# Performance work log

Hardware: AMD Instinct MI355X
Metric: run time of the kernel (lower is better)

The kernel has to match this reference:

```python
import jax, jax.numpy as jnp
import numpy as np
from jax import lax

V, E, H = 32000, 512, 1024  # vocab, embedding_dim, hidden_dim
S, B, T = 50, 64, 10        # src len, batch, max decode steps
SOS = 0


def setup_inputs() -> dict:
    key = jax.random.key(0)
    ks = jax.random.split(key, 16)
    sc = 0.02
    n = jax.random.normal
    return {
        "enc_out": n(ks[0], (S, B, 2 * H), jnp.float32),
        "hidden": n(ks[1], (1, B, H), jnp.float32),
        "target": jax.random.randint(ks[2], (B, T), 0, V),
        "emb": n(ks[3], (V, E), jnp.float32) * sc,
        "w_ih": n(ks[4], (3 * H, E), jnp.float32) * sc,
        "w_hh": n(ks[5], (3 * H, H), jnp.float32) * sc,
        "b_ih": n(ks[6], (3 * H,), jnp.float32) * sc,
        "b_hh": n(ks[7], (3 * H,), jnp.float32) * sc,
        "wa_w": n(ks[8], (H, H), jnp.float32) * sc,
        "wa_b": n(ks[9], (H,), jnp.float32) * sc,
        "ua_w": n(ks[10], (H, 2 * H), jnp.float32) * sc,
        "ua_b": n(ks[11], (H,), jnp.float32) * sc,
        "va_w": n(ks[12], (1, H), jnp.float32) * sc,
        "va_b": n(ks[13], (1,), jnp.float32) * sc,
    }


def reference(enc_out, hidden, target, emb, w_ih, w_hh, b_ih, b_hh,
              wa_w, wa_b, ua_w, ua_b, va_w, va_b):
    b, t = target.shape

    def gru_cell(x, h):
        gi = x @ w_ih.T + b_ih          # [B, 3H]
        gh = h @ w_hh.T + b_hh          # [B, 3H]
        ir, iz, inn = jnp.split(gi, 3, axis=-1)
        hr, hz, hn = jnp.split(gh, 3, axis=-1)
        r = jax.nn.sigmoid(ir + hr)
        z = jax.nn.sigmoid(iz + hz)
        nng = jnp.tanh(inn + r * hn)
        return (1.0 - z) * nng + z * h

    # teacher-forced decoder inputs: [SOS, target[:, :-1]] -> [T, B]
    dec_in = jnp.concatenate(
        [jnp.full((b, 1), SOS, dtype=target.dtype), target[:, : t - 1]], axis=1)
    xs = emb[dec_in].transpose(1, 0, 2)  # [T, B, E] (dropout is identity in eval)

    def step(h, x):
        h2 = gru_cell(x, h)
        return h2, h2

    h_last, hs = lax.scan(step, hidden[0], xs)   # hs: [T, B, H]

    keys = enc_out.transpose(1, 0, 2)            # [B, S, 2H]
    uk = keys @ ua_w.T + ua_b                    # [B, S, H]
    wq = hs @ wa_w.T + wa_b                      # [T, B, H]
    # additive (Bahdanau) scores: [T, B, S]
    scores = (jnp.tanh(wq[:, :, None, :] + uk[None]) @ va_w.T + va_b)[..., 0]
    weights = jax.nn.softmax(scores, axis=-1)    # over source positions
    context = jnp.einsum('tbs,bsd->btd', weights, keys)  # [B, T, 2H]
    out = jax.nn.log_softmax(context, axis=-1)   # [B, T, 2H]
    return out, h_last
```

## Files before the change

### kernel.cpp

```cpp
#include <hip/hip_runtime.h>
#include <math.h>

#define VOCAB 32000
#define E_DIM 512
#define H_DIM 1024
#define S_LEN 50
#define B_SZ 64
#define T_LEN 10
#define H3 (3 * H_DIM)
#define D2H (2 * H_DIM)

typedef __attribute__((ext_vector_type(8))) short short8;
typedef __attribute__((ext_vector_type(4))) float floatx4;

__device__ __forceinline__ ushort f2b(float f) {
    union { float f; uint32_t u; } x; x.f = f;
    uint32_t r = (x.u + 0x7fff + ((x.u >> 16) & 1)) >> 16;
    return (ushort)r;
}
__device__ __forceinline__ float b2f(ushort u) {
    union { float f; uint32_t u; } x; x.u = ((uint32_t)u) << 16;
    return x.f;
}
__device__ __forceinline__ float fast_sigmoid(float x) {
    x = fminf(fmaxf(x, -30.f), 30.f);
    return 1.f / (1.f + __expf(-x));
}
__device__ __forceinline__ float fast_tanh(float x) {
    x = fminf(fmaxf(x, -15.f), 15.f);
    float e = __expf(2.f * x);
    return (e - 1.f) / (e + 1.f);
}

#define PB0 1536
#define PB1 (PB0 + 3072)
#define PB2 (PB1 + 2048)
#define PB3 (PB2 + 1024)
#define PB4 (PB3 + 3200)
#define PB5 (PB4 + 640)
#define PB6 (PB5 + 64)

__device__ __forceinline__ void cvt_chunk(const float* src, ushort* dst, int i) {
    float4 v = ((const float4*)src)[i];
    ushort4 o;
    o.x = f2b(v.x); o.y = f2b(v.y); o.z = f2b(v.z); o.w = f2b(v.w);
    ((ushort4*)dst)[i] = o;
}

__global__ __launch_bounds__(256) void prep(
    const float* __restrict__ w_ih, ushort* __restrict__ w_ihb,
    const float* __restrict__ w_hh, ushort* __restrict__ w_hhb,
    const float* __restrict__ ua_w, ushort* __restrict__ ua_wb,
    const float* __restrict__ wa_w, ushort* __restrict__ wa_wb,
    const float* __restrict__ enc_out, ushort* __restrict__ keysb,
    const int* __restrict__ target, const float* __restrict__ emb,
    ushort* __restrict__ Xb,
    const float* __restrict__ hidden, float* __restrict__ h, ushort* __restrict__ hb0) {
    int bid = blockIdx.x, tid = threadIdx.x;
    if (bid < PB0) {
        cvt_chunk(w_ih, w_ihb, bid * 256 + tid);
    } else if (bid < PB1) {
        cvt_chunk(w_hh, w_hhb, (bid - PB0) * 256 + tid);
    } else if (bid < PB2) {
        cvt_chunk(ua_w, ua_wb, (bid - PB1) * 256 + tid);
    } else if (bid < PB3) {
        cvt_chunk(wa_w, wa_wb, (bid - PB2) * 256 + tid);
    } else if (bid < PB4) {
        int bs = bid - PB3;
        int b = bs / S_LEN, s = bs % S_LEN;
        const float* src = enc_out + ((size_t)s * B_SZ + b) * D2H;
        ushort* dst = keysb + (size_t)bs * D2H;
#pragma unroll
        for (int p = 0; p < 2; ++p) {
            int i = tid + p * 256;
            float4 v = ((const float4*)src)[i];
            ushort4 o;
            o.x = f2b(v.x); o.y = f2b(v.y); o.z = f2b(v.z); o.w = f2b(v.w);
            ((ushort4*)dst)[i] = o;
        }
    } else if (bid < PB5) {
        int m = bid - PB4;
        int t = m / B_SZ, b = m % B_SZ;
        int idx = (t == 0) ? 0 : target[b * T_LEN + (t - 1)];
        if (tid < 128) {
            const float* src = emb + (size_t)idx * E_DIM;
            float4 v = ((const float4*)src)[tid];
            ushort4 o;
            o.x = f2b(v.x); o.y = f2b(v.y); o.z = f2b(v.z); o.w = f2b(v.w);
            ((ushort4*)(Xb + (size_t)m * E_DIM))[tid] = o;
        }
    } else {
        int i = (bid - PB5) * 256 + tid;
        float4 v = ((const float4*)hidden)[i];
        ((float4*)h)[i] = v;
        ushort4 o;
        o.x = f2b(v.x); o.y = f2b(v.y); o.z = f2b(v.z); o.w = f2b(v.w);
        ((ushort4*)hb0)[i] = o;
    }
}

template <int BM, int WMW, int WNW>
__global__ __launch_bounds__(256) void gemm_bf16_nt(
    const ushort* __restrict__ A, const ushort* __restrict__ W,
    const float* __restrict__ bias, float* __restrict__ C,
    int M, int N, int K, int nbn) {
    constexpr int BN = 128;
    constexpr int MI = BM / (16 * WMW);
    constexpr int NI = BN / (16 * WNW);
    constexpr int AC = (BM * 4) / 256;
    constexpr int BC = (BN * 4) / 256;

    __shared__ ushort As[BM * 40];
    __shared__ ushort Bs[BN * 40];

    const int tid = threadIdx.x;
    const int w = tid >> 6, lane = tid & 63;
    const int lm = lane & 15, q = lane >> 4;
    const int wm = w / WNW, wn = w % WNW;
    const int bid = blockIdx.x;
    const int n0 = (bid % nbn) * BN;
    const int m0 = (bid / nbn) * BM;

    floatx4 acc[MI][NI];
#pragma unroll
    for (int i = 0; i < MI; ++i)
#pragma unroll
        for (int j = 0; j < NI; ++j)
            acc[i][j] = (floatx4){0.f, 0.f, 0.f, 0.f};

    short8 ar[AC], br[BC];
    auto load_tiles = [&](int k0) {
#pragma unroll
        for (int p = 0; p < AC; ++p) {
            int c = tid + p * 256;
            int row = c >> 2, qq = c & 3;
            ar[p] = *(const short8*)&A[(size_t)(m0 + row) * K + k0 + qq * 8];
        }
#pragma unroll
        for (int p = 0; p < BC; ++p) {
            int c = tid + p * 256;
            int row = c >> 2, qq = c & 3;
            br[p] = *(const short8*)&W[(size_t)(n0 + row) * K + k0 + qq * 8];
        }
    };

    load_tiles(0);
    for (int k0 = 0; k0 < K; k0 += 32) {
#pragma unroll
        for (int p = 0; p < AC; ++p) {
            int c = tid + p * 256;
            *(short8*)&As[(c >> 2) * 40 + (c & 3) * 8] = ar[p];
        }
#pragma unroll
        for (int p = 0; p < BC; ++p) {
            int c = tid + p * 256;
            *(short8*)&Bs[(c >> 2) * 40 + (c & 3) * 8] = br[p];
        }
        __syncthreads();
        if (k0 + 32 < K) load_tiles(k0 + 32);

        short8 af[MI], bfr[NI];
#pragma unroll
        for (int i = 0; i < MI; ++i)
            af[i] = *(const short8*)&As[(wm * MI * 16 + i * 16 + lm) * 40 + q * 8];
#pragma unroll
        for (int j = 0; j < NI; ++j)
            bfr[j] = *(const short8*)&Bs[(wn * NI * 16 + j * 16 + lm) * 40 + q * 8];
#pragma unroll
        for (int i = 0; i < MI; ++i)
#pragma unroll
            for (int j = 0; j < NI; ++j)
                acc[i][j] = __builtin_amdgcn_mfma_f32_16x16x32_bf16(af[i], bfr[j], acc[i][j], 0, 0, 0);
        __syncthreads();
    }

    float bv[NI];
#pragma unroll
    for (int j = 0; j < NI; ++j)
        bv[j] = bias[n0 + wn * NI * 16 + j * 16 + lm];
#pragma unroll
    for (int i = 0; i < MI; ++i) {
#pragma unroll
        for (int j = 0; j < NI; ++j) {
            int col = n0 + wn * NI * 16 + j * 16 + lm;
#pragma unroll
            for (int r = 0; r < 4; ++r) {
                int row = m0 + wm * MI * 16 + i * 16 + q * 4 + r;
                C[(size_t)row * N + col] = acc[i][j][r] + bv[j];
            }
        }
    }
}

__global__ __launch_bounds__(256) void gru_step(
    const ushort* __restrict__ hbin, const ushort* __restrict__ wb,
    const float* __restrict__ bhh, const float* __restrict__ GI,
    float* __restrict__ h, ushort* __restrict__ hbout,
    ushort* __restrict__ hsb, float* __restrict__ hlast, int t) {
    __shared__ ushort Hs[64 * 72];
    __shared__ ushort Ws[48 * 72];
    const int tid = threadIdx.x;
    const int wm = tid >> 6, lane = tid & 63;
    const int lm = lane & 15, q = lane >> 4;
    const int j0 = blockIdx.x * 16;

    floatx4 accr = {0.f, 0.f, 0.f, 0.f};
    floatx4 accz = {0.f, 0.f, 0.f, 0.f};
    floatx4 accn = {0.f, 0.f, 0.f, 0.f};

    short8 ar0, ar1, br0, br1;
    auto load_tiles = [&](int k0) {
        {
            int c = tid;
            ar0 = *(const short8*)&hbin[(size_t)(c >> 3) * H_DIM + k0 + (c & 7) * 8];
        }
        {
            int c = tid + 256;
            ar1 = *(const short8*)&hbin[(size_t)(c >> 3) * H_DIM + k0 + (c & 7) * 8];
        }
        {
            int c = tid;
            int nl = c >> 3;
            int grow = (nl >> 4) * H_DIM + j0 + (nl & 15);
            br0 = *(const short8*)&wb[(size_t)grow * H_DIM + k0 + (c & 7) * 8];
        }
        if (tid < 128) {
            int c = tid + 256;
            int nl = c >> 3;
            int grow = (nl >> 4) * H_DIM + j0 + (nl & 15);
            br1 = *(const short8*)&wb[(size_t)grow * H_DIM + k0 + (c & 7) * 8];
        }
    };

    load_tiles(0);
    for (int k0 = 0; k0 < H_DIM; k0 += 64) {
        {
            int c = tid;
            *(short8*)&Hs[(c >> 3) * 72 + (c & 7) * 8] = ar0;
        }
        {
            int c = tid + 256;
            *(short8*)&Hs[(c >> 3) * 72 + (c & 7) * 8] = ar1;
        }
        {
            int c = tid;
            *(short8*)&Ws[(c >> 3) * 72 + (c & 7) * 8] = br0;
        }
        if (tid < 128) {
            int c = tid + 256;
            *(short8*)&Ws[(c >> 3) * 72 + (c & 7) * 8] = br1;
        }
        __syncthreads();
        if (k0 + 64 < H_DIM) load_tiles(k0 + 64);
#pragma unroll
        for (int kk = 0; kk < 2; ++kk) {
            short8 af = *(const short8*)&Hs[(wm * 16 + lm) * 72 + kk * 32 + q * 8];
            short8 b0 = *(const short8*)&Ws[(lm) * 72 + kk * 32 + q * 8];
            short8 b1 = *(const short8*)&Ws[(16 + lm) * 72 + kk * 32 + q * 8];
            short8 b2 = *(const short8*)&Ws[(32 + lm) * 72 + kk * 32 + q * 8];
            accr = __builtin_amdgcn_mfma_f32_16x16x32_bf16(af, b0, accr, 0, 0, 0);
            accz = __builtin_amdgcn_mfma_f32_16x16x32_bf16(af, b1, accz, 0, 0, 0);
            accn = __builtin_amdgcn_mfma_f32_16x16x32_bf16(af, b2, accn, 0, 0, 0);
        }
        __syncthreads();
    }

    const int j = j0 + lm;
    const float bhr = bhh[j], bhz = bhh[H_DIM + j], bhn = bhh[2 * H_DIM + j];
#pragma unroll
    for (int r = 0; r < 4; ++r) {
        int b = wm * 16 + q * 4 + r;
        const float* gi = GI + (size_t)(t * B_SZ + b) * H3 + j;
        float ir = gi[0], iz = gi[H_DIM], in = gi[2 * H_DIM];
        float hr = accr[r] + bhr, hz = accz[r] + bhz, hn = accn[r] + bhn;
        float rg = fast_sigmoid(ir + hr);
        float z = fast_sigmoid(iz + hz);
        float ng = fast_tanh(in + rg * hn);
        size_t hi = (size_t)b * H_DIM + j;
        float hv = h[hi];
        float hnew = (1.f - z) * ng + z * hv;
        h[hi] = hnew;
        ushort h16 = f2b(hnew);
        hbout[hi] = h16;
        hsb[(size_t)t * B_SZ * H_DIM + hi] = h16;
        if (t == T_LEN - 1) hlast[hi] = hnew;
    }
}

__global__ __launch_bounds__(256) void attn_scores(const float* __restrict__ WQ,
                                                   const float* __restrict__ UK,
                                                   const float* __restrict__ va_w,
                                                   const float* __restrict__ va_b,
                                                   float* __restrict__ weights) {
    __shared__ float wq_s[H_DIM];
    __shared__ float va_s[H_DIM];
    __shared__ float sc[S_LEN];
    int tb = blockIdx.x;
    int b = tb % B_SZ;
    int tid = threadIdx.x;
    for (int hh = tid; hh < H_DIM; hh += 256) {
        wq_s[hh] = WQ[(size_t)tb * H_DIM + hh];
        va_s[hh] = va_w[hh];
    }
    __syncthreads();
    int wave = tid / 64, lane = tid % 64;
    for (int s = wave; s < S_LEN; s += 4) {
        const float* uk = UK + ((size_t)b * S_LEN + s) * H_DIM;
        float acc = 0.f;
#pragma unroll
        for (int i = 0; i < H_DIM / 64; ++i) {
            int hh = i * 64 + lane;
            acc += fast_tanh(wq_s[hh] + uk[hh]) * va_s[hh];
        }
        for (int off = 32; off > 0; off >>= 1) acc += __shfl_down(acc, off);
        if (lane == 0) sc[s] = acc + va_b[0];
    }
    __syncthreads();
    if (tid < 64) {
        float v = (tid < S_LEN) ? sc[tid] : -INFINITY;
        float m = v;
        for (int off = 32; off > 0; off >>= 1) m = fmaxf(m, __shfl_down(m, off));
        m = __shfl(m, 0);
        float e = (tid < S_LEN) ? __expf(v - m) : 0.f;
        float sum = e;
        for (int off = 32; off > 0; off >>= 1) sum += __shfl_down(sum, off);
        sum = __shfl(sum, 0);
        if (tid < S_LEN) weights[(size_t)tb * S_LEN + tid] = e / sum;
    }
}

__global__ __launch_bounds__(256) void ctx_logsoftmax(const float* __restrict__ weights,
                                                      const ushort* __restrict__ keysb,
                                                      float* __restrict__ out) {
    __shared__ float w_s[S_LEN];
    __shared__ float wred[4];
    __shared__ float sred[4];
    int bt = blockIdx.x;
    int t = bt >> 6, b = bt & 63;
    int tid = threadIdx.x;
    if (tid < S_LEN) w_s[tid] = weights[((size_t)t * B_SZ + b) * S_LEN + tid];
    __syncthreads();

    float c[8];
#pragma unroll
    for (int i = 0; i < 8; ++i) c[i] = 0.f;
    const ushort* kb = keysb + (size_t)b * S_LEN * D2H + tid * 8;
    for (int s = 0; s < S_LEN; ++s) {
        float ws = w_s[s];
        short8 kv = *(const short8*)&kb[(size_t)s * D2H];
#pragma unroll
        for (int i = 0; i < 8; ++i) c[i] += ws * b2f((ushort)kv[i]);
    }

    int wave = tid / 64, lane = tid % 64;
    float m = c[0];
#pragma unroll
    for (int i = 1; i < 8; ++i) m = fmaxf(m, c[i]);
    for (int off = 32; off > 0; off >>= 1) m = fmaxf(m, __shfl_down(m, off));
    if (lane == 0) wred[wave] = m;
    __syncthreads();
    if (tid == 0) wred[0] = fmaxf(fmaxf(wred[0], wred[1]), fmaxf(wred[2], wred[3]));
    __syncthreads();
    m = wred[0];
    float sum = 0.f;
#pragma unroll
    for (int i = 0; i < 8; ++i) sum += __expf(c[i] - m);
    for (int off = 32; off > 0; off >>= 1) sum += __shfl_down(sum, off);
    if (lane == 0) sred[wave] = sum;
    __syncthreads();
    if (tid == 0) sred[0] = sred[0] + sred[1] + sred[2] + sred[3];
    __syncthreads();
    float lse = m + __logf(sred[0]);

    float* o = out + ((size_t)b * T_LEN + t) * D2H + tid * 8;
#pragma unroll
    for (int i = 0; i < 8; ++i) o[i] = c[i] - lse;
}

extern "C" void kernel_launch(void* const* d_in, const int* in_sizes, int n_in,
                              void* d_out, int out_size, void* d_ws, size_t ws_size,
                              hipStream_t stream) {
    const float* enc_out = (const float*)d_in[0];
    const float* hidden  = (const float*)d_in[1];
    const int*   target  = (const int*)d_in[2];
    const float* emb     = (const float*)d_in[3];
    const float* w_ih    = (const float*)d_in[4];
    const float* w_hh    = (const float*)d_in[5];
    const float* b_ih    = (const float*)d_in[6];
    const float* b_hh    = (const float*)d_in[7];
    const float* wa_w    = (const float*)d_in[8];
    const float* wa_b    = (const float*)d_in[9];
    const float* ua_w    = (const float*)d_in[10];
    const float* ua_b    = (const float*)d_in[11];
    const float* va_w    = (const float*)d_in[12];
    const float* va_b    = (const float*)d_in[13];
    float* out = (float*)d_out;

    const int TB = T_LEN * B_SZ;
    const int BS = B_SZ * S_LEN;

    char* p = (char*)d_ws;
    float*  GI    = (float*)p;  p += (size_t)TB * H3 * 4;
    float*  UK    = (float*)p;  p += (size_t)BS * H_DIM * 4;
    float*  WQ    = (float*)p;  p += (size_t)TB * H_DIM * 4;
    float*  h     = (float*)p;  p += (size_t)B_SZ * H_DIM * 4;
    float*  wts   = (float*)p;  p += (size_t)TB * S_LEN * 4;
    p = (char*)(((uintptr_t)p + 255) & ~(uintptr_t)255);
    ushort* keysb = (ushort*)p; p += (size_t)BS * D2H * 2;
    ushort* Xb    = (ushort*)p; p += (size_t)TB * E_DIM * 2;
    ushort* w_ihb = (ushort*)p; p += (size_t)H3 * E_DIM * 2;
    ushort* w_hhb = (ushort*)p; p += (size_t)H3 * H_DIM * 2;
    ushort* ua_wb = (ushort*)p; p += (size_t)H_DIM * D2H * 2;
    ushort* wa_wb = (ushort*)p; p += (size_t)H_DIM * H_DIM * 2;
    ushort* hb0   = (ushort*)p; p += (size_t)B_SZ * H_DIM * 2;
    ushort* hb1   = (ushort*)p; p += (size_t)B_SZ * H_DIM * 2;
    ushort* hsb   = (ushort*)p; p += (size_t)TB * H_DIM * 2;

    prep<<<PB6, 256, 0, stream>>>(w_ih, w_ihb, w_hh, w_hhb, ua_w, ua_wb, wa_w, wa_wb,
                                  enc_out, keysb, target, emb, Xb, hidden, h, hb0);

    gemm_bf16_nt<128, 2, 2><<<(TB / 128) * (H3 / 128), 256, 0, stream>>>(
        Xb, w_ihb, b_ih, GI, TB, H3, E_DIM, H3 / 128);
    gemm_bf16_nt<128, 2, 2><<<(BS / 128) * (H_DIM / 128), 256, 0, stream>>>(
        keysb, ua_wb, ua_b, UK, BS, H_DIM, D2H, H_DIM / 128);

    float* hlast = out + (size_t)B_SZ * T_LEN * D2H;
    for (int t = 0; t < T_LEN; ++t) {
        const ushort* hin = (t & 1) ? hb1 : hb0;
        ushort* hout = (t & 1) ? hb0 : hb1;
        gru_step<<<B_SZ, 256, 0, stream>>>(hin, w_hhb, b_hh, GI, h, hout, hsb, hlast, t);
    }

    gemm_bf16_nt<128, 2, 2><<<(TB / 128) * (H_DIM / 128), 256, 0, stream>>>(
        hsb, wa_wb, wa_b, WQ, TB, H_DIM, H_DIM, H_DIM / 128);

    attn_scores<<<TB, 256, 0, stream>>>(WQ, UK, va_w, va_b, wts);

    ctx_logsoftmax<<<B_SZ * T_LEN, 256, 0, stream>>>(wts, keysb, out);
}
```

Before: 370.6 us.

## Persistent GRU kernel with grid barrier, merged GEMMs, fused attention, bf16 intermediates

Replaces the ten per-step GRU launches with one persistent kernel of 64 blocks that sync through an atomic grid barrier. The hidden state stays in registers and the W_hh tiles are double-buffered in LDS. The two input GEMMs run as one launch with a new 64x128 tile and K-step of 64, and UK and WQ are stored as bf16. Attention scores, softmax and context/log-softmax are fused into one kernel, which removes launch overhead and intermediate traffic. The grid barrier relies on all 64 blocks being co-resident, and the bf16 intermediates add rounding error.

```diff
diff --git a/kernel.cpp b/kernel.cpp
--- a/kernel.cpp
+++ b/kernel.cpp
@@ -55,8 +55,10 @@
     const float* __restrict__ enc_out, ushort* __restrict__ keysb,
     const int* __restrict__ target, const float* __restrict__ emb,
     ushort* __restrict__ Xb,
-    const float* __restrict__ hidden, float* __restrict__ h, ushort* __restrict__ hb0) {
+    const float* __restrict__ hidden, ushort* __restrict__ hb0,
+    int* __restrict__ bar) {
     int bid = blockIdx.x, tid = threadIdx.x;
+    if (bid == 0 && tid < 8) bar[tid] = 0;
     if (bid < PB0) {
         cvt_chunk(w_ih, w_ihb, bid * 256 + tid);
     } else if (bid < PB1) {
@@ -90,232 +92,257 @@
             ((ushort4*)(Xb + (size_t)m * E_DIM))[tid] = o;
         }
     } else {
-        int i = (bid - PB5) * 256 + tid;
-        float4 v = ((const float4*)hidden)[i];
-        ((float4*)h)[i] = v;
-        ushort4 o;
-        o.x = f2b(v.x); o.y = f2b(v.y); o.z = f2b(v.z); o.w = f2b(v.w);
-        ((ushort4*)hb0)[i] = o;
-    }
-}
-
-template <int BM, int WMW, int WNW>
-__global__ __launch_bounds__(256) void gemm_bf16_nt(
-    const ushort* __restrict__ A, const ushort* __restrict__ W,
-    const float* __restrict__ bias, float* __restrict__ C,
-    int M, int N, int K, int nbn) {
-    constexpr int BN = 128;
-    constexpr int MI = BM / (16 * WMW);
-    constexpr int NI = BN / (16 * WNW);
-    constexpr int AC = (BM * 4) / 256;
-    constexpr int BC = (BN * 4) / 256;
-
-    __shared__ ushort As[BM * 40];
-    __shared__ ushort Bs[BN * 40];
+        cvt_chunk(hidden, hb0, (bid - PB5) * 256 + tid);
+    }
+}
+
+struct GemmArgs {
+    const ushort* A; const ushort* W; const float* bias;
+    float* Cf; ushort* C16;
+    int M, N, K, nbn, nblk;
+};
+
+__global__ __launch_bounds__(256) void gemm_bf16(GemmArgs g0, GemmArgs g1) {
+    const bool first = (int)blockIdx.x < g0.nblk;
+    GemmArgs g = first ? g0 : g1;
+    const int bid = first ? blockIdx.x : (blockIdx.x - g0.nblk);
+
+    __shared__ ushort As[64 * 72];
+    __shared__ ushort Bs[128 * 72];
 
     const int tid = threadIdx.x;
     const int w = tid >> 6, lane = tid & 63;
     const int lm = lane & 15, q = lane >> 4;
-    const int wm = w / WNW, wn = w % WNW;
-    const int bid = blockIdx.x;
-    const int n0 = (bid % nbn) * BN;
-    const int m0 = (bid / nbn) * BM;
-
-    floatx4 acc[MI][NI];
-#pragma unroll
-    for (int i = 0; i < MI; ++i)
-#pragma unroll
-        for (int j = 0; j < NI; ++j)
+    const int wm = w >> 1, wn = w & 1;
+    const int n0 = (bid % g.nbn) * 128;
+    const int m0 = (bid / g.nbn) * 64;
+    const int K = g.K;
+
+    floatx4 acc[2][4];
+#pragma unroll
+    for (int i = 0; i < 2; ++i)
+#pragma unroll
+        for (int j = 0; j < 4; ++j)
             acc[i][j] = (floatx4){0.f, 0.f, 0.f, 0.f};
 
-    short8 ar[AC], br[BC];
+    short8 ar[2], br[4];
     auto load_tiles = [&](int k0) {
 #pragma unroll
-        for (int p = 0; p < AC; ++p) {
-            int c = tid + p * 256;
-            int row = c >> 2, qq = c & 3;
-            ar[p] = *(const short8*)&A[(size_t)(m0 + row) * K + k0 + qq * 8];
-        }
-#pragma unroll
-        for (int p = 0; p < BC; ++p) {
-            int c = tid + p * 256;
-            int row = c >> 2, qq = c & 3;
-            br[p] = *(const short8*)&W[(size_t)(n0 + row) * K + k0 + qq * 8];
+        for (int p = 0; p < 2; ++p) {
+            int c = tid + p * 256;
+            ar[p] = *(const short8*)&g.A[(size_t)(m0 + (c >> 3)) * K + k0 + (c & 7) * 8];
+        }
+#pragma unroll
+        for (int p = 0; p < 4; ++p) {
+            int c = tid + p * 256;
+            br[p] = *(const short8*)&g.W[(size_t)(n0 + (c >> 3)) * K + k0 + (c & 7) * 8];
         }
     };
 
     load_tiles(0);
-    for (int k0 = 0; k0 < K; k0 += 32) {
-#pragma unroll
-        for (int p = 0; p < AC; ++p) {
-            int c = tid + p * 256;
-            *(short8*)&As[(c >> 2) * 40 + (c & 3) * 8] = ar[p];
-        }
-#pragma unroll
-        for (int p = 0; p < BC; ++p) {
-            int c = tid + p * 256;
-            *(short8*)&Bs[(c >> 2) * 40 + (c & 3) * 8] = br[p];
+    for (int k0 = 0; k0 < K; k0 += 64) {
+#pragma unroll
+        for (int p = 0; p < 2; ++p) {
+            int c = tid + p * 256;
+            *(short8*)&As[(c >> 3) * 72 + (c & 7) * 8] = ar[p];
+        }
+#pragma unroll
+        for (int p = 0; p < 4; ++p) {
+            int c = tid + p * 256;
+            *(short8*)&Bs[(c >> 3) * 72 + (c & 7) * 8] = br[p];
         }
         __syncthreads();
-        if (k0 + 32 < K) load_tiles(k0 + 32);
-
-        short8 af[MI], bfr[NI];
-#pragma unroll
-        for (int i = 0; i < MI; ++i)
-            af[i] = *(const short8*)&As[(wm * MI * 16 + i * 16 + lm) * 40 + q * 8];
-#pragma unroll
-        for (int j = 0; j < NI; ++j)
-            bfr[j] = *(const short8*)&Bs[(wn * NI * 16 + j * 16 + lm) * 40 + q * 8];
-#pragma unroll
-        for (int i = 0; i < MI; ++i)
-#pragma unroll
-            for (int j = 0; j < NI; ++j)
-                acc[i][j] = __builtin_amdgcn_mfma_f32_16x16x32_bf16(af[i], bfr[j], acc[i][j], 0, 0, 0);
+        if (k0 + 64 < K) load_tiles(k0 + 64);
+
+#pragma unroll
+        for (int kk = 0; kk < 2; ++kk) {
+            short8 af[2], bf[4];
+#pragma unroll
+            for (int i = 0; i < 2; ++i)
+                af[i] = *(const short8*)&As[(wm * 32 + i * 16 + lm) * 72 + kk * 32 + q * 8];
+#pragma unroll
+            for (int j = 0; j < 4; ++j)
+                bf[j] = *(const short8*)&Bs[(wn * 64 + j * 16 + lm) * 72 + kk * 32 + q * 8];
+#pragma unroll
+            for (int i = 0; i < 2; ++i)
+#pragma unroll
+                for (int j = 0; j < 4; ++j)
+                    acc[i][j] = __builtin_amdgcn_mfma_f32_16x16x32_bf16(af[i], bf[j], acc[i][j], 0, 0, 0);
+        }
         __syncthreads();
     }
 
-    float bv[NI];
-#pragma unroll
-    for (int j = 0; j < NI; ++j)
-        bv[j] = bias[n0 + wn * NI * 16 + j * 16 + lm];
-#pragma unroll
-    for (int i = 0; i < MI; ++i) {
-#pragma unroll
-        for (int j = 0; j < NI; ++j) {
-            int col = n0 + wn * NI * 16 + j * 16 + lm;
+    float bv[4];
+#pragma unroll
+    for (int j = 0; j < 4; ++j)
+        bv[j] = g.bias[n0 + wn * 64 + j * 16 + lm];
+#pragma unroll
+    for (int i = 0; i < 2; ++i) {
+#pragma unroll
+        for (int j = 0; j < 4; ++j) {
+            int col = n0 + wn * 64 + j * 16 + lm;
 #pragma unroll
             for (int r = 0; r < 4; ++r) {
-                int row = m0 + wm * MI * 16 + i * 16 + q * 4 + r;
-                C[(size_t)row * N + col] = acc[i][j][r] + bv[j];
+                int row = m0 + wm * 32 + i * 16 + q * 4 + r;
+                float v = acc[i][j][r] + bv[j];
+                if (g.C16) g.C16[(size_t)row * g.N + col] = f2b(v);
+                else       g.Cf[(size_t)row * g.N + col] = v;
             }
         }
     }
 }
 
-__global__ __launch_bounds__(256) void gru_step(
-    const ushort* __restrict__ hbin, const ushort* __restrict__ wb,
-    const float* __restrict__ bhh, const float* __restrict__ GI,
-    float* __restrict__ h, ushort* __restrict__ hbout,
-    ushort* __restrict__ hsb, float* __restrict__ hlast, int t) {
-    __shared__ ushort Hs[64 * 72];
-    __shared__ ushort Ws[48 * 72];
+#define GRU_BLOCKS 64
+
+__device__ __forceinline__ void grid_barrier(int* cnt, int* gen, int phase) {
+    __syncthreads();
+    if (threadIdx.x == 0) {
+        __threadfence();
+        if (atomicAdd(cnt, 1) == GRU_BLOCKS - 1) {
+            atomicExch(cnt, 0);
+            __threadfence();
+            atomicExch(gen, phase + 1);
+        } else {
+            while (atomicAdd(gen, 0) <= phase) __builtin_amdgcn_s_sleep(8);
+        }
+        __threadfence();
+    }
+    __syncthreads();
+}
+
+__global__ __launch_bounds__(256) void gru_persistent(
+    const ushort* __restrict__ w_hhb, const float* __restrict__ bhh,
+    const float* __restrict__ GI, const float* __restrict__ hidden,
+    ushort* __restrict__ hb0, ushort* __restrict__ hb1,
+    ushort* __restrict__ hsb, float* __restrict__ outTail,
+    int* __restrict__ bar) {
+    __shared__ ushort Ws[2][48 * 136];
     const int tid = threadIdx.x;
-    const int wm = tid >> 6, lane = tid & 63;
+    const int w = tid >> 6, lane = tid & 63;
     const int lm = lane & 15, q = lane >> 4;
     const int j0 = blockIdx.x * 16;
-
-    floatx4 accr = {0.f, 0.f, 0.f, 0.f};
-    floatx4 accz = {0.f, 0.f, 0.f, 0.f};
-    floatx4 accn = {0.f, 0.f, 0.f, 0.f};
-
-    short8 ar0, ar1, br0, br1;
-    auto load_tiles = [&](int k0) {
-        {
-            int c = tid;
-            ar0 = *(const short8*)&hbin[(size_t)(c >> 3) * H_DIM + k0 + (c & 7) * 8];
-        }
-        {
-            int c = tid + 256;
-            ar1 = *(const short8*)&hbin[(size_t)(c >> 3) * H_DIM + k0 + (c & 7) * 8];
-        }
-        {
-            int c = tid;
-            int nl = c >> 3;
-            int grow = (nl >> 4) * H_DIM + j0 + (nl & 15);
-            br0 = *(const short8*)&wb[(size_t)grow * H_DIM + k0 + (c & 7) * 8];
-        }
-        if (tid < 128) {
-            int c = tid + 256;
-            int nl = c >> 3;
-            int grow = (nl >> 4) * H_DIM + j0 + (nl & 15);
-            br1 = *(const short8*)&wb[(size_t)grow * H_DIM + k0 + (c & 7) * 8];
+    const int j = j0 + lm;
+
+    const float bhr = bhh[j], bhz = bhh[H_DIM + j], bhn = bhh[2 * H_DIM + j];
+
+    float hf[4];
+#pragma unroll
+    for (int r = 0; r < 4; ++r)
+        hf[r] = hidden[(size_t)(w * 16 + q * 4 + r) * H_DIM + j];
+
+    short8 wr[3];
+    auto stage_regs = [&](int kbase) {
+#pragma unroll
+        for (int p = 0; p < 3; ++p) {
+            int c = tid + p * 256;
+            int row = c >> 4, off = c & 15;
+            int grow = (row >> 4) * H_DIM + j0 + (row & 15);
+            wr[p] = *(const short8*)&w_hhb[(size_t)grow * H_DIM + kbase + off * 8];
         }
     };
-
-    load_tiles(0);
-    for (int k0 = 0; k0 < H_DIM; k0 += 64) {
-        {
-            int c = tid;
-            *(short8*)&Hs[(c >> 3) * 72 + (c & 7) * 8] = ar0;
-        }
-        {
-            int c = tid + 256;
-            *(short8*)&Hs[(c >> 3) * 72 + (c & 7) * 8] = ar1;
-        }
-        {
-            int c = tid;
-            *(short8*)&Ws[(c >> 3) * 72 + (c & 7) * 8] = br0;
-        }
-        if (tid < 128) {
-            int c = tid + 256;
-            *(short8*)&Ws[(c >> 3) * 72 + (c & 7) * 8] = br1;
-        }
-        __syncthreads();
-        if (k0 + 64 < H_DIM) load_tiles(k0 + 64);
-#pragma unroll
-        for (int kk = 0; kk < 2; ++kk) {
-            short8 af = *(const short8*)&Hs[(wm * 16 + lm) * 72 + kk * 32 + q * 8];
-            short8 b0 = *(const short8*)&Ws[(lm) * 72 + kk * 32 + q * 8];
-            short8 b1 = *(const short8*)&Ws[(16 + lm) * 72 + kk * 32 + q * 8];
-            short8 b2 = *(const short8*)&Ws[(32 + lm) * 72 + kk * 32 + q * 8];
-            accr = __builtin_amdgcn_mfma_f32_16x16x32_bf16(af, b0, accr, 0, 0, 0);
-            accz = __builtin_amdgcn_mfma_f32_16x16x32_bf16(af, b1, accz, 0, 0, 0);
-            accn = __builtin_amdgcn_mfma_f32_16x16x32_bf16(af, b2, accn, 0, 0, 0);
-        }
-        __syncthreads();
-    }
-
-    const int j = j0 + lm;
-    const float bhr = bhh[j], bhz = bhh[H_DIM + j], bhn = bhh[2 * H_DIM + j];
-#pragma unroll
-    for (int r = 0; r < 4; ++r) {
-        int b = wm * 16 + q * 4 + r;
-        const float* gi = GI + (size_t)(t * B_SZ + b) * H3 + j;
-        float ir = gi[0], iz = gi[H_DIM], in = gi[2 * H_DIM];
-        float hr = accr[r] + bhr, hz = accz[r] + bhz, hn = accn[r] + bhn;
-        float rg = fast_sigmoid(ir + hr);
-        float z = fast_sigmoid(iz + hz);
-        float ng = fast_tanh(in + rg * hn);
-        size_t hi = (size_t)b * H_DIM + j;
-        float hv = h[hi];
-        float hnew = (1.f - z) * ng + z * hv;
-        h[hi] = hnew;
-        ushort h16 = f2b(hnew);
-        hbout[hi] = h16;
-        hsb[(size_t)t * B_SZ * H_DIM + hi] = h16;
-        if (t == T_LEN - 1) hlast[hi] = hnew;
-    }
-}
-
-__global__ __launch_bounds__(256) void attn_scores(const float* __restrict__ WQ,
-                                                   const float* __restrict__ UK,
-                                                   const float* __restrict__ va_w,
-                                                   const float* __restrict__ va_b,
-                                                   float* __restrict__ weights) {
+    auto write_lds = [&](int buf) {
+#pragma unroll
+        for (int p = 0; p < 3; ++p) {
+            int c = tid + p * 256;
+            *(short8*)&Ws[buf][(c >> 4) * 136 + (c & 15) * 8] = wr[p];
+        }
+    };
+
+    for (int t = 0; t < T_LEN; ++t) {
+        const ushort* hin = (t & 1) ? hb1 : hb0;
+        ushort* hout = (t & 1) ? hb0 : hb1;
+
+        float ir[4], iz[4], inn[4];
+#pragma unroll
+        for (int r = 0; r < 4; ++r) {
+            const float* gi = GI + (size_t)(t * B_SZ + w * 16 + q * 4 + r) * H3 + j;
+            ir[r] = gi[0]; iz[r] = gi[H_DIM]; inn[r] = gi[2 * H_DIM];
+        }
+
+        floatx4 accr = {0.f, 0.f, 0.f, 0.f};
+        floatx4 accz = {0.f, 0.f, 0.f, 0.f};
+        floatx4 accn = {0.f, 0.f, 0.f, 0.f};
+
+        stage_regs(0);
+        write_lds(0);
+        const ushort* arow = hin + (size_t)(w * 16 + lm) * H_DIM + q * 8;
+
+        for (int it = 0; it < 8; ++it) {
+            __syncthreads();
+            if (it < 7) stage_regs((it + 1) * 128);
+            short8 af[4];
+#pragma unroll
+            for (int kk = 0; kk < 4; ++kk)
+                af[kk] = *(const short8*)&arow[it * 128 + kk * 32];
+            const int buf = it & 1;
+#pragma unroll
+            for (int kk = 0; kk < 4; ++kk) {
+                short8 b0 = *(const short8*)&Ws[buf][(lm) * 136 + kk * 32 + q * 8];
+                short8 b1 = *(const short8*)&Ws[buf][(16 + lm) * 136 + kk * 32 + q * 8];
+                short8 b2 = *(const short8*)&Ws[buf][(32 + lm) * 136 + kk * 32 + q * 8];
+                accr = __builtin_amdgcn_mfma_f32_16x16x32_bf16(af[kk], b0, accr, 0, 0, 0);
+                accz = __builtin_amdgcn_mfma_f32_16x16x32_bf16(af[kk], b1, accz, 0, 0, 0);
+                accn = __builtin_amdgcn_mfma_f32_16x16x32_bf16(af[kk], b2, accn, 0, 0, 0);
+            }
+            if (it < 7) write_lds(buf ^ 1);
+        }
+
+#pragma unroll
+        for (int r = 0; r < 4; ++r) {
+            int b = w * 16 + q * 4 + r;
+            float rg = fast_sigmoid(ir[r] + accr[r] + bhr);
+            float z  = fast_sigmoid(iz[r] + accz[r] + bhz);
+            float ng = fast_tanh(inn[r] + rg * (accn[r] + bhn));
+            float hnew = (1.f - z) * ng + z * hf[r];
+            hf[r] = hnew;
+            size_t hi = (size_t)b * H_DIM + j;
+            ushort h16 = f2b(hnew);
+            hout[hi] = h16;
+            hsb[(size_t)t * B_SZ * H_DIM + hi] = h16;
+            if (t == T_LEN - 1) outTail[hi] = hnew;
+        }
+
+        if (t < T_LEN - 1) grid_barrier(&bar[0], &bar[1], t);
+    }
+}
+
+__global__ __launch_bounds__(256) void attn_ctx(
+    const ushort* __restrict__ WQ16, const ushort* __restrict__ UK16,
+    const float* __restrict__ va_w, const float* __restrict__ va_b,
+    const ushort* __restrict__ keysb, float* __restrict__ out) {
     __shared__ float wq_s[H_DIM];
     __shared__ float va_s[H_DIM];
     __shared__ float sc[S_LEN];
-    int tb = blockIdx.x;
-    int b = tb % B_SZ;
-    int tid = threadIdx.x;
+    __shared__ float wred[4];
+    __shared__ float sred[4];
+    const int bt = blockIdx.x;
+    const int t = bt >> 6, b = bt & 63;
+    const int tid = threadIdx.x;
+    const int wave = tid >> 6, lane = tid & 63;
+
     for (int hh = tid; hh < H_DIM; hh += 256) {
-        wq_s[hh] = WQ[(size_t)tb * H_DIM + hh];
+        wq_s[hh] = b2f(WQ16[(size_t)(t * B_SZ + b) * H_DIM + hh]);
         va_s[hh] = va_w[hh];
     }
     __syncthreads();
-    int wave = tid / 64, lane = tid % 64;
+
     for (int s = wave; s < S_LEN; s += 4) {
-        const float* uk = UK + ((size_t)b * S_LEN + s) * H_DIM;
+        const ushort* uk = UK16 + ((size_t)b * S_LEN + s) * H_DIM + lane * 16;
+        short8 u0 = *(const short8*)&uk[0];
+        short8 u1 = *(const short8*)&uk[8];
         float acc = 0.f;
-#pragma unroll
-        for (int i = 0; i < H_DIM / 64; ++i) {
-            int hh = i * 64 + lane;
-            acc += fast_tanh(wq_s[hh] + uk[hh]) * va_s[hh];
-        }
+        const int h0 = lane * 16;
+#pragma unroll
+        for (int i = 0; i < 8; ++i)
+            acc += fast_tanh(wq_s[h0 + i] + b2f((ushort)u0[i])) * va_s[h0 + i];
+#pragma unroll
+        for (int i = 0; i < 8; ++i)
+            acc += fast_tanh(wq_s[h0 + 8 + i] + b2f((ushort)u1[i])) * va_s[h0 + 8 + i];
         for (int off = 32; off > 0; off >>= 1) acc += __shfl_down(acc, off);
         if (lane == 0) sc[s] = acc + va_b[0];
     }
     __syncthreads();
+
     if (tid < 64) {
         float v = (tid < S_LEN) ? sc[tid] : -INFINITY;
         float m = v;
@@ -325,20 +352,8 @@
         float sum = e;
         for (int off = 32; off > 0; off >>= 1) sum += __shfl_down(sum, off);
         sum = __shfl(sum, 0);
-        if (tid < S_LEN) weights[(size_t)tb * S_LEN + tid] = e / sum;
-    }
-}
-
-__global__ __launch_bounds__(256) void ctx_logsoftmax(const float* __restrict__ weights,
-                                                      const ushort* __restrict__ keysb,
-                                                      float* __restrict__ out) {
-    __shared__ float w_s[S_LEN];
-    __shared__ float wred[4];
-    __shared__ float sred[4];
-    int bt = blockIdx.x;
-    int t = bt >> 6, b = bt & 63;
-    int tid = threadIdx.x;
-    if (tid < S_LEN) w_s[tid] = weights[((size_t)t * B_SZ + b) * S_LEN + tid];
+        if (tid < S_LEN) sc[tid] = e / sum;
+    }
     __syncthreads();
 
     float c[8];
@@ -346,13 +361,12 @@
     for (int i = 0; i < 8; ++i) c[i] = 0.f;
     const ushort* kb = keysb + (size_t)b * S_LEN * D2H + tid * 8;
     for (int s = 0; s < S_LEN; ++s) {
-        float ws = w_s[s];
+        float ws = sc[s];
         short8 kv = *(const short8*)&kb[(size_t)s * D2H];
 #pragma unroll
         for (int i = 0; i < 8; ++i) c[i] += ws * b2f((ushort)kv[i]);
     }
 
-    int wave = tid / 64, lane = tid % 64;
     float m = c[0];
 #pragma unroll
     for (int i = 1; i < 8; ++i) m = fmaxf(m, c[i]);
@@ -400,11 +414,8 @@
     const int BS = B_SZ * S_LEN;
 
     char* p = (char*)d_ws;
+    int*    bar   = (int*)p;    p += 256;
     float*  GI    = (float*)p;  p += (size_t)TB * H3 * 4;
-    float*  UK    = (float*)p;  p += (size_t)BS * H_DIM * 4;
-    float*  WQ    = (float*)p;  p += (size_t)TB * H_DIM * 4;
-    float*  h     = (float*)p;  p += (size_t)B_SZ * H_DIM * 4;
-    float*  wts   = (float*)p;  p += (size_t)TB * S_LEN * 4;
     p = (char*)(((uintptr_t)p + 255) & ~(uintptr_t)255);
     ushort* keysb = (ushort*)p; p += (size_t)BS * D2H * 2;
     ushort* Xb    = (ushort*)p; p += (size_t)TB * E_DIM * 2;
@@ -415,26 +426,25 @@
     ushort* hb0   = (ushort*)p; p += (size_t)B_SZ * H_DIM * 2;
     ushort* hb1   = (ushort*)p; p += (size_t)B_SZ * H_DIM * 2;
     ushort* hsb   = (ushort*)p; p += (size_t)TB * H_DIM * 2;
+    ushort* UK16  = (ushort*)p; p += (size_t)BS * H_DIM * 2;
+    ushort* WQ16  = (ushort*)p; p += (size_t)TB * H_DIM * 2;
 
     prep<<<PB6, 256, 0, stream>>>(w_ih, w_ihb, w_hh, w_hhb, ua_w, ua_wb, wa_w, wa_wb,
-                                  enc_out, keysb, target, emb, Xb, hidden, h, hb0);
-
-    gemm_bf16_nt<128, 2, 2><<<(TB / 128) * (H3 / 128), 256, 0, stream>>>(
-        Xb, w_ihb, b_ih, GI, TB, H3, E_DIM, H3 / 128);
-    gemm_bf16_nt<128, 2, 2><<<(BS / 128) * (H_DIM / 128), 256, 0, stream>>>(
-        keysb, ua_wb, ua_b, UK, BS, H_DIM, D2H, H_DIM / 128);
-
-    float* hlast = out + (size_t)B_SZ * T_LEN * D2H;
-    for (int t = 0; t < T_LEN; ++t) {
-        const ushort* hin = (t & 1) ? hb1 : hb0;
-        ushort* hout = (t & 1) ? hb0 : hb1;
-        gru_step<<<B_SZ, 256, 0, stream>>>(hin, w_hhb, b_hh, GI, h, hout, hsb, hlast, t);
-    }
-
-    gemm_bf16_nt<128, 2, 2><<<(TB / 128) * (H_DIM / 128), 256, 0, stream>>>(
-        hsb, wa_wb, wa_b, WQ, TB, H_DIM, H_DIM, H_DIM / 128);
-
-    attn_scores<<<TB, 256, 0, stream>>>(WQ, UK, va_w, va_b, wts);
-
-    ctx_logsoftmax<<<B_SZ * T_LEN, 256, 0, stream>>>(wts, keysb, out);
-}
+                                  enc_out, keysb, target, emb, Xb, hidden, hb0, bar);
+
+    GemmArgs guk = { keysb, ua_wb, ua_b, nullptr, UK16,
+                     BS, H_DIM, D2H, H_DIM / 128, (BS / 64) * (H_DIM / 128) };
+    GemmArgs ggi = { Xb, w_ihb, b_ih, GI, nullptr,
+                     TB, H3, E_DIM, H3 / 128, (TB / 64) * (H3 / 128) };
+    gemm_bf16<<<guk.nblk + ggi.nblk, 256, 0, stream>>>(guk, ggi);
+
+    float* outTail = out + (size_t)B_SZ * T_LEN * D2H;
+    gru_persistent<<<GRU_BLOCKS, 256, 0, stream>>>(w_hhb, b_hh, GI, hidden,
+                                                   hb0, hb1, hsb, outTail, bar);
+
+    GemmArgs gwq = { hsb, wa_wb, wa_b, nullptr, WQ16,
+                     TB, H_DIM, H_DIM, H_DIM / 128, (TB / 64) * (H_DIM / 128) };
+    gemm_bf16<<<gwq.nblk, 256, 0, stream>>>(gwq, gwq);
+
+    attn_ctx<<<B_SZ * T_LEN, 256, 0, stream>>>(WQ16, UK16, va_w, va_b, keysb, out);
+}
```

After: 355.8 us. 4.0% less time.
